# Kernel tuning notes

Measured on AMD Instinct MI355X. Metric: run time of the kernel, lower is better.

## Reference

```python
import jax, jax.numpy as jnp
import numpy as np

NUM_INSTANCES = 64  # instance ids in [0, 64); id 0 is background and excluded


def _variance_smooth_loss(variances, ins_labels, num_segments):
    # variances: [N, D] float, ins_labels: [N] int
    N, D = variances.shape
    ones = jnp.ones((N,), dtype=variances.dtype)
    counts = jax.ops.segment_sum(ones, ins_labels, num_segments=num_segments)          # [S]
    sums = jax.ops.segment_sum(variances, ins_labels, num_segments=num_segments)       # [S, D]
    safe_counts = jnp.maximum(counts, 1.0)
    means = sums / safe_counts[:, None]                                                # per-instance mean [S, D]
    diff = variances - means[ins_labels]                                               # gather means back [N, D]
    sq = jnp.sum(diff * diff, axis=1)                                                  # [N]
    # per-instance MSE = sum of squared diffs / (K_i * D), matching nn.MSELoss (mean reduction)
    per_ins = jax.ops.segment_sum(sq, ins_labels, num_segments=num_segments) / (safe_counts * D)
    valid = (counts > 0) & (jnp.arange(num_segments) != 0)                             # skip id 0 & absent ids
    return jnp.sum(jnp.where(valid, per_ins, jnp.zeros_like(per_ins)))


def setup_inputs() -> dict:
    key = jax.random.key(0)
    k1, k2 = jax.random.split(key)
    N, D = 4_000_000, 8
    variances = jax.random.normal(k1, (N, D), dtype=jnp.float32)
    ins_labels = jax.random.randint(k2, (N,), 0, NUM_INSTANCES, dtype=jnp.int32)
    return {"variances": variances, "ins_labels": ins_labels}


def reference(variances, ins_labels):
    return _variance_smooth_loss(variances, ins_labels, NUM_INSTANCES)
```

## Files before the change

### kernel.cpp

```cpp
#include <hip/hip_runtime.h>

#define NUM_INST 64
#define SLOT 12
#define BLOCK 256
#define NWAVES 4
#define GRID 1024

__global__ __launch_bounds__(BLOCK) void vsl_main(const float4* __restrict__ rows,
                                                  const int* __restrict__ labels,
                                                  float* __restrict__ gacc, int n) {
    __shared__ float lds[NWAVES][NUM_INST * SLOT];
    const int tid = threadIdx.x;
    const int w = tid >> 6;
    const int lane = tid & 63;

    float s0 = 0, s1 = 0, s2 = 0, s3 = 0, s4 = 0, s5 = 0, s6 = 0, s7 = 0;
    float ssq = 0, cntf = 0;

    float* slotbase = &lds[w][lane * SLOT];
    const int stride = GRID * BLOCK;

    for (int i = blockIdx.x * BLOCK + tid;; i += stride) {
        const bool valid = (i < n);
        const unsigned long long bv = __ballot(valid);
        if (!bv) break;

        int lbl = 0;
        float4 a = {0, 0, 0, 0}, b = {0, 0, 0, 0};
        if (valid) {
            lbl = labels[i];
            a = rows[2 * i];
            b = rows[2 * i + 1];
        }

        *(float4*)(slotbase) = a;
        *(float4*)(slotbase + 4) = b;

        unsigned long long m = bv;
#pragma unroll
        for (int bpos = 0; bpos < 6; ++bpos) {
            const unsigned long long bb = __ballot((lbl >> bpos) & 1);
            m &= ((lane >> bpos) & 1) ? bb : ~bb;
        }
        cntf += (float)__popcll(m);

        asm volatile("s_waitcnt lgkmcnt(0)" ::: "memory");

        while (m) {
            const int s = (int)__builtin_ctzll(m);
            m &= m - 1;
            const float* sp = &lds[w][s * SLOT];
            const float4 p = *(const float4*)sp;
            const float4 q = *(const float4*)(sp + 4);
            s0 += p.x; s1 += p.y; s2 += p.z; s3 += p.w;
            s4 += q.x; s5 += q.y; s6 += q.z; s7 += q.w;
            ssq += p.x * p.x + p.y * p.y + p.z * p.z + p.w * p.w +
                   q.x * q.x + q.y * q.y + q.z * q.z + q.w * q.w;
        }
    }

    float* fb = &lds[w][lane * SLOT];
    fb[0] = s0; fb[1] = s1; fb[2] = s2; fb[3] = s3;
    fb[4] = s4; fb[5] = s5; fb[6] = s6; fb[7] = s7;
    fb[8] = ssq; fb[9] = cntf;
    __syncthreads();

    for (int j = tid; j < NUM_INST * 10; j += BLOCK) {
        const int lbl = j / 10;
        const int st = j - lbl * 10;
        float v = 0;
#pragma unroll
        for (int ww = 0; ww < NWAVES; ++ww) v += lds[ww][lbl * SLOT + st];
        atomicAdd(&gacc[j], v);
    }
}

__global__ __launch_bounds__(64) void vsl_final(const float* __restrict__ gacc,
                                                float* __restrict__ out) {
    const int s = threadIdx.x;
    float val = 0.0f;
    const float* base = &gacc[s * 10];
    const float cnt = base[9];
    if (s != 0 && cnt > 0.0f) {
        const float ss = base[8];
        float m2 = 0.0f;
#pragma unroll
        for (int d = 0; d < 8; ++d) {
            const float sd = base[d];
            m2 += sd * sd;
        }
        val = (ss - m2 / cnt) / (cnt * 8.0f);
    }
#pragma unroll
    for (int off = 32; off > 0; off >>= 1) val += __shfl_down(val, off, 64);
    if (s == 0) out[0] = val;
}

extern "C" void kernel_launch(void* const* d_in, const int* in_sizes, int n_in,
                              void* d_out, int out_size, void* d_ws, size_t ws_size,
                              hipStream_t stream) {
    const float* variances = (const float*)d_in[0];
    const int* labels = (const int*)d_in[1];
    const int n = in_sizes[1];
    float* gacc = (float*)d_ws;

    hipMemsetAsync(d_ws, 0, NUM_INST * 10 * sizeof(float), stream);
    vsl_main<<<GRID, BLOCK, 0, stream>>>((const float4*)variances, labels, gacc, n);
    vsl_final<<<1, 64, 0, stream>>>(gacc, (float*)d_out);
}
```

Baseline: 211.6 us.

## Replace ballot-based wave histogram with LDS float atomics per label

Drops the per-wave ballot label matching and serial per-lane LDS gather loop. Each thread now adds its row's sums, sum of squares and count straight into a single block-shared per-label accumulator using LDS atomicAdd, with a stride of 11 to spread banks. This removes the six ballots and the variable-length serial loop per iteration. The cost is ten LDS atomics per row, contended across the whole block over only 64 labels, and float atomic ordering makes the accumulation order nondeterministic.

```diff
diff --git a/kernel.cpp b/kernel.cpp
--- a/kernel.cpp
+++ b/kernel.cpp
@@ -1,77 +1,50 @@
 #include <hip/hip_runtime.h>
 
 #define NUM_INST 64
-#define SLOT 12
+#define ASLOT 11
 #define BLOCK 256
-#define NWAVES 4
 #define GRID 1024
 
 __global__ __launch_bounds__(BLOCK) void vsl_main(const float4* __restrict__ rows,
                                                   const int* __restrict__ labels,
                                                   float* __restrict__ gacc, int n) {
-    __shared__ float lds[NWAVES][NUM_INST * SLOT];
-    const int tid = threadIdx.x;
-    const int w = tid >> 6;
-    const int lane = tid & 63;
-
-    float s0 = 0, s1 = 0, s2 = 0, s3 = 0, s4 = 0, s5 = 0, s6 = 0, s7 = 0;
-    float ssq = 0, cntf = 0;
-
-    float* slotbase = &lds[w][lane * SLOT];
-    const int stride = GRID * BLOCK;
-
-    for (int i = blockIdx.x * BLOCK + tid;; i += stride) {
-        const bool valid = (i < n);
-        const unsigned long long bv = __ballot(valid);
-        if (!bv) break;
-
-        int lbl = 0;
-        float4 a = {0, 0, 0, 0}, b = {0, 0, 0, 0};
-        if (valid) {
-            lbl = labels[i];
-            a = rows[2 * i];
-            b = rows[2 * i + 1];
-        }
-
-        *(float4*)(slotbase) = a;
-        *(float4*)(slotbase + 4) = b;
-
-        unsigned long long m = bv;
-#pragma unroll
-        for (int bpos = 0; bpos < 6; ++bpos) {
-            const unsigned long long bb = __ballot((lbl >> bpos) & 1);
-            m &= ((lane >> bpos) & 1) ? bb : ~bb;
-        }
-        cntf += (float)__popcll(m);
-
-        asm volatile("s_waitcnt lgkmcnt(0)" ::: "memory");
-
-        while (m) {
-            const int s = (int)__builtin_ctzll(m);
-            m &= m - 1;
-            const float* sp = &lds[w][s * SLOT];
-            const float4 p = *(const float4*)sp;
-            const float4 q = *(const float4*)(sp + 4);
-            s0 += p.x; s1 += p.y; s2 += p.z; s3 += p.w;
-            s4 += q.x; s5 += q.y; s6 += q.z; s7 += q.w;
-            ssq += p.x * p.x + p.y * p.y + p.z * p.z + p.w * p.w +
-                   q.x * q.x + q.y * q.y + q.z * q.z + q.w * q.w;
-        }
-    }
-
-    float* fb = &lds[w][lane * SLOT];
-    fb[0] = s0; fb[1] = s1; fb[2] = s2; fb[3] = s3;
-    fb[4] = s4; fb[5] = s5; fb[6] = s6; fb[7] = s7;
-    fb[8] = ssq; fb[9] = cntf;
+    __shared__ float acc[NUM_INST * ASLOT];
+    for (int j = threadIdx.x; j < NUM_INST * ASLOT; j += BLOCK) acc[j] = 0.0f;
     __syncthreads();
 
-    for (int j = tid; j < NUM_INST * 10; j += BLOCK) {
+    const int stride = GRID * BLOCK;
+    for (int i = blockIdx.x * BLOCK + threadIdx.x; i < n; i += stride) {
+        const int lbl = labels[i];
+        const float4 a = rows[2 * i];
+        const float4 b = rows[2 * i + 1];
+
+        float ssq = a.x * a.x;
+        ssq = fmaf(a.y, a.y, ssq);
+        ssq = fmaf(a.z, a.z, ssq);
+        ssq = fmaf(a.w, a.w, ssq);
+        ssq = fmaf(b.x, b.x, ssq);
+        ssq = fmaf(b.y, b.y, ssq);
+        ssq = fmaf(b.z, b.z, ssq);
+        ssq = fmaf(b.w, b.w, ssq);
+
+        float* s = &acc[lbl * ASLOT];
+        atomicAdd(&s[0], a.x);
+        atomicAdd(&s[1], a.y);
+        atomicAdd(&s[2], a.z);
+        atomicAdd(&s[3], a.w);
+        atomicAdd(&s[4], b.x);
+        atomicAdd(&s[5], b.y);
+        atomicAdd(&s[6], b.z);
+        atomicAdd(&s[7], b.w);
+        atomicAdd(&s[8], ssq);
+        atomicAdd(&s[9], 1.0f);
+    }
+    __syncthreads();
+
+    for (int j = threadIdx.x; j < NUM_INST * 10; j += BLOCK) {
         const int lbl = j / 10;
         const int st = j - lbl * 10;
-        float v = 0;
-#pragma unroll
-        for (int ww = 0; ww < NWAVES; ++ww) v += lds[ww][lbl * SLOT + st];
-        atomicAdd(&gacc[j], v);
+        atomicAdd(&gacc[j], acc[lbl * ASLOT + st]);
     }
 }
 
```

Measured after the change: 346.5 us. 1.64x slower.

## Software-pipeline global loads and LDS reads, precompute row sum of squares

Applied to the files above, without the earlier changes.

Global loads for the next grid-stride iteration are now issued before the current row is processed, so memory latency overlaps with the LDS label-matching work. Each thread computes its own row's sum of squares once and stores it in the LDS slot, so the consumer lane no longer recomputes eight squares per gathered row. The inner gather loop is double-buffered so the next LDS read is issued before the current one is accumulated, and the explicit lgkmcnt wait is removed. The grid is doubled for more waves in flight. The cost is more live registers, which may lower occupancy, and twice as many blocks doing the final global atomics.

```diff
diff --git a/kernel.cpp b/kernel.cpp
--- a/kernel.cpp
+++ b/kernel.cpp
@@ -4,7 +4,7 @@
 #define SLOT 12
 #define BLOCK 256
 #define NWAVES 4
-#define GRID 1024
+#define GRID 2048
 
 __global__ __launch_bounds__(BLOCK) void vsl_main(const float4* __restrict__ rows,
                                                   const int* __restrict__ labels,
@@ -20,21 +20,37 @@
     float* slotbase = &lds[w][lane * SLOT];
     const int stride = GRID * BLOCK;
 
-    for (int i = blockIdx.x * BLOCK + tid;; i += stride) {
-        const bool valid = (i < n);
-        const unsigned long long bv = __ballot(valid);
-        if (!bv) break;
+    int i = blockIdx.x * BLOCK + tid;
+    bool valid = (i < n);
+    unsigned long long bv = __ballot(valid);
+    int lbl = 0;
+    float4 a = {0, 0, 0, 0}, b = {0, 0, 0, 0};
+    if (valid) {
+        lbl = labels[i];
+        a = rows[2 * i];
+        b = rows[2 * i + 1];
+    }
 
-        int lbl = 0;
-        float4 a = {0, 0, 0, 0}, b = {0, 0, 0, 0};
-        if (valid) {
-            lbl = labels[i];
-            a = rows[2 * i];
-            b = rows[2 * i + 1];
+    while (bv) {
+        const int inext = i + stride;
+        const bool vnext = (inext < n);
+        const unsigned long long bvn = __ballot(vnext);
+        int lbln = 0;
+        float4 an = {0, 0, 0, 0}, bn = {0, 0, 0, 0};
+        if (vnext) {
+            lbln = labels[inext];
+            an = rows[2 * inext];
+            bn = rows[2 * inext + 1];
         }
+
+        float sq = a.x * a.x;
+        sq = fmaf(a.y, a.y, sq); sq = fmaf(a.z, a.z, sq); sq = fmaf(a.w, a.w, sq);
+        sq = fmaf(b.x, b.x, sq); sq = fmaf(b.y, b.y, sq);
+        sq = fmaf(b.z, b.z, sq); sq = fmaf(b.w, b.w, sq);
 
         *(float4*)(slotbase) = a;
         *(float4*)(slotbase + 4) = b;
+        slotbase[8] = sq;
 
         unsigned long long m = bv;
 #pragma unroll
@@ -44,19 +60,36 @@
         }
         cntf += (float)__popcll(m);
 
-        asm volatile("s_waitcnt lgkmcnt(0)" ::: "memory");
-
-        while (m) {
-            const int s = (int)__builtin_ctzll(m);
+        int g = -1;
+        float4 p = {0, 0, 0, 0}, q = {0, 0, 0, 0};
+        float r = 0;
+        if (m) {
+            g = (int)__builtin_ctzll(m);
             m &= m - 1;
-            const float* sp = &lds[w][s * SLOT];
-            const float4 p = *(const float4*)sp;
-            const float4 q = *(const float4*)(sp + 4);
+            const float* sp = &lds[w][g * SLOT];
+            p = *(const float4*)sp;
+            q = *(const float4*)(sp + 4);
+            r = sp[8];
+        }
+        while (g >= 0) {
+            int g2 = -1;
+            float4 p2 = {0, 0, 0, 0}, q2 = {0, 0, 0, 0};
+            float r2 = 0;
+            if (m) {
+                g2 = (int)__builtin_ctzll(m);
+                m &= m - 1;
+                const float* sp = &lds[w][g2 * SLOT];
+                p2 = *(const float4*)sp;
+                q2 = *(const float4*)(sp + 4);
+                r2 = sp[8];
+            }
             s0 += p.x; s1 += p.y; s2 += p.z; s3 += p.w;
             s4 += q.x; s5 += q.y; s6 += q.z; s7 += q.w;
-            ssq += p.x * p.x + p.y * p.y + p.z * p.z + p.w * p.w +
-                   q.x * q.x + q.y * q.y + q.z * q.z + q.w * q.w;
+            ssq += r;
+            g = g2; p = p2; q = q2; r = r2;
         }
+
+        i = inext; bv = bvn; lbl = lbln; a = an; b = bn;
     }
 
     float* fb = &lds[w][lane * SLOT];
@@ -66,11 +99,11 @@
     __syncthreads();
 
     for (int j = tid; j < NUM_INST * 10; j += BLOCK) {
-        const int lbl = j / 10;
-        const int st = j - lbl * 10;
+        const int lbl2 = j / 10;
+        const int st = j - lbl2 * 10;
         float v = 0;
 #pragma unroll
-        for (int ww = 0; ww < NWAVES; ++ww) v += lds[ww][lbl * SLOT + st];
+        for (int ww = 0; ww < NWAVES; ++ww) v += lds[ww][lbl2 * SLOT + st];
         atomicAdd(&gacc[j], v);
     }
 }
```

After: 227.6 us. 1.08x slower.

## Process two rows per thread per phase and precompute squared norms before LDS transpose

Applied to the files above, without the earlier changes.

Each thread now loads two rows per loop iteration (two grid-strided chunks) so more global loads are in flight at once, and the grid grows from 1024 to 1536 blocks. The per-row sum of squares is computed by the owning lane and stored in the LDS slot, so the lane that accumulates for a label adds one value instead of redoing eight multiplies. The LDS buffer doubles in size, which may reduce occupancy, and the gather loop gains branching to choose between the two slot sets.

```diff
diff --git a/kernel.cpp b/kernel.cpp
--- a/kernel.cpp
+++ b/kernel.cpp
@@ -4,12 +4,13 @@
 #define SLOT 12
 #define BLOCK 256
 #define NWAVES 4
-#define GRID 1024
+#define GRID 1536
+#define RCH 2
 
 __global__ __launch_bounds__(BLOCK) void vsl_main(const float4* __restrict__ rows,
                                                   const int* __restrict__ labels,
                                                   float* __restrict__ gacc, int n) {
-    __shared__ float lds[NWAVES][NUM_INST * SLOT];
+    __shared__ float lds[NWAVES][RCH * NUM_INST * SLOT];
     const int tid = threadIdx.x;
     const int w = tid >> 6;
     const int lane = tid & 63;
@@ -17,45 +18,70 @@
     float s0 = 0, s1 = 0, s2 = 0, s3 = 0, s4 = 0, s5 = 0, s6 = 0, s7 = 0;
     float ssq = 0, cntf = 0;
 
-    float* slotbase = &lds[w][lane * SLOT];
-    const int stride = GRID * BLOCK;
+    const int S = GRID * BLOCK;
+    const int phaseStride = RCH * S;
+    const int nphases = (n + phaseStride - 1) / phaseStride;
 
-    for (int i = blockIdx.x * BLOCK + tid;; i += stride) {
-        const bool valid = (i < n);
-        const unsigned long long bv = __ballot(valid);
-        if (!bv) break;
+    float* slot0 = &lds[w][lane * SLOT];
+    float* slot1 = &lds[w][(NUM_INST + lane) * SLOT];
 
-        int lbl = 0;
-        float4 a = {0, 0, 0, 0}, b = {0, 0, 0, 0};
-        if (valid) {
-            lbl = labels[i];
-            a = rows[2 * i];
-            b = rows[2 * i + 1];
-        }
+    int i0 = blockIdx.x * BLOCK + tid;
 
-        *(float4*)(slotbase) = a;
-        *(float4*)(slotbase + 4) = b;
+    for (int ph = 0; ph < nphases; ++ph, i0 += phaseStride) {
+        const int i1 = i0 + S;
+        const bool v0 = (i0 < n);
+        const bool v1 = (i1 < n);
 
-        unsigned long long m = bv;
+        int l0 = 0, l1 = 0;
+        float4 a0 = {0, 0, 0, 0}, b0 = {0, 0, 0, 0};
+        float4 a1 = {0, 0, 0, 0}, b1 = {0, 0, 0, 0};
+        if (v0) { l0 = labels[i0]; a0 = rows[2 * i0]; b0 = rows[2 * i0 + 1]; }
+        if (v1) { l1 = labels[i1]; a1 = rows[2 * i1]; b1 = rows[2 * i1 + 1]; }
+
+        float q0 = a0.x * a0.x;
+        q0 = fmaf(a0.y, a0.y, q0); q0 = fmaf(a0.z, a0.z, q0); q0 = fmaf(a0.w, a0.w, q0);
+        q0 = fmaf(b0.x, b0.x, q0); q0 = fmaf(b0.y, b0.y, q0);
+        q0 = fmaf(b0.z, b0.z, q0); q0 = fmaf(b0.w, b0.w, q0);
+        float q1 = a1.x * a1.x;
+        q1 = fmaf(a1.y, a1.y, q1); q1 = fmaf(a1.z, a1.z, q1); q1 = fmaf(a1.w, a1.w, q1);
+        q1 = fmaf(b1.x, b1.x, q1); q1 = fmaf(b1.y, b1.y, q1);
+        q1 = fmaf(b1.z, b1.z, q1); q1 = fmaf(b1.w, b1.w, q1);
+
+        *(float4*)(slot0) = a0;
+        *(float4*)(slot0 + 4) = b0;
+        slot0[8] = q0;
+        *(float4*)(slot1) = a1;
+        *(float4*)(slot1 + 4) = b1;
+        slot1[8] = q1;
+
+        const unsigned long long bv0 = __ballot(v0);
+        const unsigned long long bv1 = __ballot(v1);
+        unsigned long long m0 = bv0, m1 = bv1;
 #pragma unroll
         for (int bpos = 0; bpos < 6; ++bpos) {
-            const unsigned long long bb = __ballot((lbl >> bpos) & 1);
-            m &= ((lane >> bpos) & 1) ? bb : ~bb;
+            const unsigned long long t0 = __ballot((l0 >> bpos) & 1);
+            const unsigned long long t1 = __ballot((l1 >> bpos) & 1);
+            const bool mybit = (lane >> bpos) & 1;
+            m0 &= mybit ? t0 : ~t0;
+            m1 &= mybit ? t1 : ~t1;
         }
-        cntf += (float)__popcll(m);
+        cntf += (float)(__popcll(m0) + __popcll(m1));
 
         asm volatile("s_waitcnt lgkmcnt(0)" ::: "memory");
 
-        while (m) {
-            const int s = (int)__builtin_ctzll(m);
-            m &= m - 1;
-            const float* sp = &lds[w][s * SLOT];
+        while (m0 | m1) {
+            const bool use0 = (m0 != 0);
+            unsigned long long mc = use0 ? m0 : m1;
+            const int s = (int)__builtin_ctzll(mc);
+            mc &= mc - 1;
+            if (use0) m0 = mc; else m1 = mc;
+            const float* sp = &lds[w][((use0 ? 0 : NUM_INST) + s) * SLOT];
             const float4 p = *(const float4*)sp;
             const float4 q = *(const float4*)(sp + 4);
+            const float r = sp[8];
             s0 += p.x; s1 += p.y; s2 += p.z; s3 += p.w;
             s4 += q.x; s5 += q.y; s6 += q.z; s7 += q.w;
-            ssq += p.x * p.x + p.y * p.y + p.z * p.z + p.w * p.w +
-                   q.x * q.x + q.y * q.y + q.z * q.z + q.w * q.w;
+            ssq += r;
         }
     }
 
@@ -66,11 +92,11 @@
     __syncthreads();
 
     for (int j = tid; j < NUM_INST * 10; j += BLOCK) {
-        const int lbl = j / 10;
-        const int st = j - lbl * 10;
+        const int lbl2 = j / 10;
+        const int st = j - lbl2 * 10;
         float v = 0;
 #pragma unroll
-        for (int ww = 0; ww < NWAVES; ++ww) v += lds[ww][lbl * SLOT + st];
+        for (int ww = 0; ww < NWAVES; ++ww) v += lds[ww][lbl2 * SLOT + st];
         atomicAdd(&gacc[j], v);
     }
 }
```

After: 212.4 us. About the same (+0.4%).
